# Performance work log

Measured on AMD Instinct MI355X. Metric: run time of the kernel, lower is better.

The kernel has to match this reference:

```python
import jax, jax.numpy as jnp
import numpy as np

B, P, S, H, R = 32, 512, 1024, 1024, 256


def setup_inputs() -> dict:
    key = jax.random.key(0)
    k1, k2, k3 = jax.random.split(key, 3)
    pairs = jax.random.randint(k1, (B, P, 2, 2), 0, S, dtype=jnp.int64 if jax.config.jax_enable_x64 else jnp.int32)
    hidden_states = jax.random.normal(k2, (B, S, H), dtype=jnp.float32)
    W = jax.random.normal(k3, (R, 3 * H), dtype=jnp.float32) * (1.0 / np.sqrt(3 * H))
    b = jnp.zeros((R,), dtype=jnp.float32)
    return {"pairs": pairs, "hidden_states": hidden_states, "W": W, "b": b}


def reference(pairs, hidden_states, W, b):
    # pairs: [B, P, 2, 2] -> [:, :, 0, :] = (h_start, h_end), [:, :, 1, :] = (t_start, t_end)
    def gather_tokens(idx):  # idx: [B, P] -> [B, P, H]
        return jnp.take_along_axis(hidden_states, idx[:, :, None], axis=1)

    head_embed = 0.5 * (gather_tokens(pairs[:, :, 0, 0]) + gather_tokens(pairs[:, :, 0, 1]))
    tail_embed = 0.5 * (gather_tokens(pairs[:, :, 1, 0]) + gather_tokens(pairs[:, :, 1, 1]))
    feats = jnp.concatenate([head_embed, tail_embed, head_embed * tail_embed], axis=-1)  # [B, P, 3H]
    logits = jnp.einsum('bpf,rf->bpr', feats, W) + b  # [B, P, R]
    return logits
```

## Files before the change

kernel.cpp:

```cpp
#include <hip/hip_runtime.h>

#define NB 32
#define NP 512
#define NS 1024
#define NH 1024
#define NR 256
#define K3 3072

#define BM 64
#define BK 64

typedef short short8 __attribute__((ext_vector_type(8)));
typedef short short4v __attribute__((ext_vector_type(4)));
typedef __bf16 bf16x8 __attribute__((ext_vector_type(8)));
typedef float f32x4 __attribute__((ext_vector_type(4)));

__device__ __forceinline__ unsigned short f2bf(float f) {
  unsigned u = __builtin_bit_cast(unsigned, f);
  u += 0x7fffu + ((u >> 16) & 1u);
  return (unsigned short)(u >> 16);
}

__device__ __forceinline__ f32x4 mfma_bf16(short8 a, short8 b, f32x4 c) {
  return __builtin_amdgcn_mfma_f32_16x16x32_bf16(
      __builtin_bit_cast(bf16x8, a), __builtin_bit_cast(bf16x8, b), c, 0, 0, 0);
}

__global__ void wconv_kernel(const float* __restrict__ W,
                             unsigned short* __restrict__ WbF) {
  int i = blockIdx.x * blockDim.x + threadIdx.x;
  int lane = i & 63, n16 = (i >> 6) & 15, kc = i >> 10;
  int lr = lane & 15, lg = lane >> 4;
  const float* src = W + (size_t)(n16 * 16 + lr) * K3 + kc * 32 + lg * 8;
  float4 a = *(const float4*)src;
  float4 b = *(const float4*)(src + 4);
  short8 o;
  o[0] = (short)f2bf(a.x); o[1] = (short)f2bf(a.y);
  o[2] = (short)f2bf(a.z); o[3] = (short)f2bf(a.w);
  o[4] = (short)f2bf(b.x); o[5] = (short)f2bf(b.y);
  o[6] = (short)f2bf(b.z); o[7] = (short)f2bf(b.w);
  *(short8*)(WbF + (size_t)i * 8) = o;
}

__global__ __launch_bounds__(512, 2) void gemm_kernel(
    const int* __restrict__ pairs, const float* __restrict__ hs,
    const unsigned short* __restrict__ WbF, const float* __restrict__ bias,
    float* __restrict__ out) {
  __shared__ __align__(16) unsigned short sA[2][3][BM][64];

  const int tid = threadIdx.x;
  const int blk = blockIdx.x;
  const int x     = blk & 7;
  const int jb    = blk >> 3;
  const int batch = x * 4 + (jb >> 3);
  const int mtile = jb & 7;
  const int m0    = (batch * 8 + mtile) * BM;

  const int pairi = tid >> 3;
  const int q     = tid & 7;
  int4 pr = ((const int4*)pairs)[m0 + pairi];
  const float* hb = hs + (size_t)batch * NS * NH;
  const float* rp[4];
  rp[0] = hb + (size_t)pr.x * NH + 4 * q;
  rp[1] = hb + (size_t)pr.y * NH + 4 * q;
  rp[2] = hb + (size_t)pr.z * NH + 4 * q;
  rp[3] = hb + (size_t)pr.w * NH + 4 * q;

  const int lane = tid & 63;
  const int w    = tid >> 6;
  const int lr   = lane & 15;
  const int lg   = lane >> 4;

  const unsigned short* wbase = WbF + (size_t)(w * 2) * 512 + (size_t)lane * 8;

  f32x4 acc[4][2];
#pragma unroll
  for (int i = 0; i < 4; ++i)
#pragma unroll
    for (int j = 0; j < 2; ++j) acc[i][j] = (f32x4){0.f, 0.f, 0.f, 0.f};

  float4 ld[8];
  short8 wcur[12], wnxt[12];

  auto load_w = [&](int s, short8* wd) {
#pragma unroll
    for (int part = 0; part < 3; ++part)
#pragma unroll
      for (int ks = 0; ks < 2; ++ks)
#pragma unroll
        for (int j = 0; j < 2; ++j)
          wd[part * 4 + ks * 2 + j] = *(const short8*)(
              wbase + (size_t)(part * 32 + s * 2 + ks) * 8192 + (size_t)j * 512);
  };

  auto load_gather = [&](int s) {
    const int o = s * BK;
#pragma unroll
    for (int jj = 0; jj < 8; ++jj)
      ld[jj] = *(const float4*)(rp[jj >> 1] + o + 32 * (jj & 1));
  };

  auto store_stage = [&](int buf) {
#pragma unroll
    for (int c = 0; c < 2; ++c) {
      short4v hv, tv, pv;
#pragma unroll
      for (int e = 0; e < 4; ++e) {
        float h = 0.5f * (((const float*)&ld[0 + c])[e] + ((const float*)&ld[2 + c])[e]);
        float t = 0.5f * (((const float*)&ld[4 + c])[e] + ((const float*)&ld[6 + c])[e]);
        float p = h * t;
        hv[e] = (short)f2bf(h); tv[e] = (short)f2bf(t); pv[e] = (short)f2bf(p);
      }
      const int chunkI = (q >> 1) + 4 * c;
      const int col = ((chunkI ^ (pairi & 7)) * 8) + (q & 1) * 4;
      *(short4v*)&sA[buf][0][pairi][col] = hv;
      *(short4v*)&sA[buf][1][pairi][col] = tv;
      *(short4v*)&sA[buf][2][pairi][col] = pv;
    }
  };

  auto compute = [&](int buf, short8* wc) {
#pragma unroll
    for (int ks = 0; ks < 2; ++ks) {
      short8 ah[4], at4[4], ap[4];
      const int col = (((ks * 4 + lg) ^ (lr & 7)) * 8);
#pragma unroll
      for (int i = 0; i < 4; ++i) {
        ah[i]  = *(const short8*)&sA[buf][0][i * 16 + lr][col];
        at4[i] = *(const short8*)&sA[buf][1][i * 16 + lr][col];
        ap[i]  = *(const short8*)&sA[buf][2][i * 16 + lr][col];
      }
#pragma unroll
      for (int j = 0; j < 2; ++j)
#pragma unroll
        for (int i = 0; i < 4; ++i) {
          acc[i][j] = mfma_bf16(ah[i],  wc[0 + ks * 2 + j], acc[i][j]);
          acc[i][j] = mfma_bf16(at4[i], wc[4 + ks * 2 + j], acc[i][j]);
          acc[i][j] = mfma_bf16(ap[i],  wc[8 + ks * 2 + j], acc[i][j]);
        }
    }
  };

  load_w(0, wcur);
  load_gather(0);
  store_stage(0);

  auto stage = [&](int s, short8* wc, short8* wn) {
    __syncthreads();
    const int buf = s & 1;
    if (s < 15) {
      load_w(s + 1, wn);
      load_gather(s + 1);
    }
    compute(buf, wc);
    if (s < 15) store_stage(buf ^ 1);
  };

#pragma unroll 1
  for (int sp = 0; sp < 8; ++sp) {
    stage(2 * sp,     wcur, wnxt);
    stage(2 * sp + 1, wnxt, wcur);
  }

#pragma unroll
  for (int j = 0; j < 2; ++j) {
    const int col  = w * 32 + j * 16 + lr;
    const float bv = bias[col];
#pragma unroll
    for (int i = 0; i < 4; ++i) {
      const size_t rbase = (size_t)(m0 + i * 16 + lg * 4) * NR + col;
#pragma unroll
      for (int r = 0; r < 4; ++r)
        out[rbase + (size_t)r * NR] = acc[i][j][r] + bv;
    }
  }
}

extern "C" void kernel_launch(void* const* d_in, const int* in_sizes, int n_in,
                              void* d_out, int out_size, void* d_ws, size_t ws_size,
                              hipStream_t stream) {
  const int*   pairs = (const int*)d_in[0];
  const float* hs    = (const float*)d_in[1];
  const float* W     = (const float*)d_in[2];
  const float* bias  = (const float*)d_in[3];
  float* out = (float*)d_out;
  unsigned short* WbF = (unsigned short*)d_ws;

  wconv_kernel<<<(96 * 16 * 64) / 256, 256, 0, stream>>>(W, WbF);
  gemm_kernel<<<(NB * NP) / BM, 512, 0, stream>>>(pairs, hs, WbF, bias, out);
}
```

Before: 231.9 us.

## Double threads per GEMM block and deepen gather prefetch to two stages

Each block now runs 1024 threads (16 waves) instead of 512, so every wave owns one 16-column N tile instead of two, and each thread gathers one float4 per row instead of two. This halves per-thread register use for accumulators and weight fragments. The gather is also prefetched two stages ahead using ping-ponged register buffers, to hide the latency of the random hidden-state loads. The cost is a heavier __syncthreads across 16 waves and each wave re-reading the shared-memory A tiles, which doubles LDS read traffic per MFMA.

Result: faster. 225.4 us (-2.8%).

```diff
diff --git a/kernel.cpp b/kernel.cpp
--- a/kernel.cpp
+++ b/kernel.cpp
@@ -42,7 +42,7 @@
   *(short8*)(WbF + (size_t)i * 8) = o;
 }
 
-__global__ __launch_bounds__(512, 2) void gemm_kernel(
+__global__ __launch_bounds__(1024, 4) void gemm_kernel(
     const int* __restrict__ pairs, const float* __restrict__ hs,
     const unsigned short* __restrict__ WbF, const float* __restrict__ bias,
     float* __restrict__ out) {
@@ -56,8 +56,8 @@
   const int mtile = jb & 7;
   const int m0    = (batch * 8 + mtile) * BM;
 
-  const int pairi = tid >> 3;
-  const int q     = tid & 7;
+  const int pairi = tid >> 4;
+  const int q     = tid & 15;
   int4 pr = ((const int4*)pairs)[m0 + pairi];
   const float* hb = hs + (size_t)batch * NS * NH;
   const float* rp[4];
@@ -71,52 +71,44 @@
   const int lr   = lane & 15;
   const int lg   = lane >> 4;
 
-  const unsigned short* wbase = WbF + (size_t)(w * 2) * 512 + (size_t)lane * 8;
+  const unsigned short* wbase = WbF + (size_t)w * 512 + (size_t)lane * 8;
 
-  f32x4 acc[4][2];
+  f32x4 acc[4];
 #pragma unroll
-  for (int i = 0; i < 4; ++i)
-#pragma unroll
-    for (int j = 0; j < 2; ++j) acc[i][j] = (f32x4){0.f, 0.f, 0.f, 0.f};
+  for (int i = 0; i < 4; ++i) acc[i] = (f32x4){0.f, 0.f, 0.f, 0.f};
 
-  float4 ld[8];
-  short8 wcur[12], wnxt[12];
+  float4 ldA[4], ldB[4];
+  short8 wcur[6], wnxt[6];
 
   auto load_w = [&](int s, short8* wd) {
 #pragma unroll
     for (int part = 0; part < 3; ++part)
 #pragma unroll
       for (int ks = 0; ks < 2; ++ks)
-#pragma unroll
-        for (int j = 0; j < 2; ++j)
-          wd[part * 4 + ks * 2 + j] = *(const short8*)(
-              wbase + (size_t)(part * 32 + s * 2 + ks) * 8192 + (size_t)j * 512);
+        wd[part * 2 + ks] = *(const short8*)(
+            wbase + (size_t)(part * 32 + s * 2 + ks) * 8192);
   };
 
-  auto load_gather = [&](int s) {
-    const int o = s * BK;
+  auto load_gather = [&](int s, float4* ld) {
 #pragma unroll
-    for (int jj = 0; jj < 8; ++jj)
-      ld[jj] = *(const float4*)(rp[jj >> 1] + o + 32 * (jj & 1));
+    for (int r = 0; r < 4; ++r)
+      ld[r] = *(const float4*)(rp[r] + s * BK);
   };
 
-  auto store_stage = [&](int buf) {
+  auto store_stage = [&](int buf, float4* ld) {
+    short4v hv, tv, pv;
 #pragma unroll
-    for (int c = 0; c < 2; ++c) {
-      short4v hv, tv, pv;
-#pragma unroll
-      for (int e = 0; e < 4; ++e) {
-        float h = 0.5f * (((const float*)&ld[0 + c])[e] + ((const float*)&ld[2 + c])[e]);
-        float t = 0.5f * (((const float*)&ld[4 + c])[e] + ((const float*)&ld[6 + c])[e]);
-        float p = h * t;
-        hv[e] = (short)f2bf(h); tv[e] = (short)f2bf(t); pv[e] = (short)f2bf(p);
-      }
-      const int chunkI = (q >> 1) + 4 * c;
-      const int col = ((chunkI ^ (pairi & 7)) * 8) + (q & 1) * 4;
-      *(short4v*)&sA[buf][0][pairi][col] = hv;
-      *(short4v*)&sA[buf][1][pairi][col] = tv;
-      *(short4v*)&sA[buf][2][pairi][col] = pv;
+    for (int e = 0; e < 4; ++e) {
+      float h = 0.5f * (((const float*)&ld[0])[e] + ((const float*)&ld[1])[e]);
+      float t = 0.5f * (((const float*)&ld[2])[e] + ((const float*)&ld[3])[e]);
+      float p = h * t;
+      hv[e] = (short)f2bf(h); tv[e] = (short)f2bf(t); pv[e] = (short)f2bf(p);
     }
+    const int chunkI = q >> 1;
+    const int col = ((chunkI ^ (pairi & 7)) * 8) + (q & 1) * 4;
+    *(short4v*)&sA[buf][0][pairi][col] = hv;
+    *(short4v*)&sA[buf][1][pairi][col] = tv;
+    *(short4v*)&sA[buf][2][pairi][col] = pv;
   };
 
   auto compute = [&](int buf, short8* wc) {
@@ -131,48 +123,41 @@
         ap[i]  = *(const short8*)&sA[buf][2][i * 16 + lr][col];
       }
 #pragma unroll
-      for (int j = 0; j < 2; ++j)
-#pragma unroll
-        for (int i = 0; i < 4; ++i) {
-          acc[i][j] = mfma_bf16(ah[i],  wc[0 + ks * 2 + j], acc[i][j]);
-          acc[i][j] = mfma_bf16(at4[i], wc[4 + ks * 2 + j], acc[i][j]);
-          acc[i][j] = mfma_bf16(ap[i],  wc[8 + ks * 2 + j], acc[i][j]);
-        }
+      for (int i = 0; i < 4; ++i) {
+        acc[i] = mfma_bf16(ah[i],  wc[0 + ks], acc[i]);
+        acc[i] = mfma_bf16(at4[i], wc[2 + ks], acc[i]);
+        acc[i] = mfma_bf16(ap[i],  wc[4 + ks], acc[i]);
+      }
     }
   };
 
+  load_gather(0, ldA);
   load_w(0, wcur);
-  load_gather(0);
-  store_stage(0);
+  store_stage(0, ldA);
+  load_gather(1, ldA);
 
-  auto stage = [&](int s, short8* wc, short8* wn) {
+  auto stage = [&](int s, short8* wc, short8* wn, float4* ldc, float4* ldn) {
     __syncthreads();
-    const int buf = s & 1;
-    if (s < 15) {
-      load_w(s + 1, wn);
-      load_gather(s + 1);
-    }
-    compute(buf, wc);
-    if (s < 15) store_stage(buf ^ 1);
+    if (s < 15) load_w(s + 1, wn);
+    if (s < 14) load_gather(s + 2, ldn);
+    compute(s & 1, wc);
+    if (s < 15) store_stage((s & 1) ^ 1, ldc);
   };
 
 #pragma unroll 1
   for (int sp = 0; sp < 8; ++sp) {
-    stage(2 * sp,     wcur, wnxt);
-    stage(2 * sp + 1, wnxt, wcur);
+    stage(2 * sp,     wcur, wnxt, ldA, ldB);
+    stage(2 * sp + 1, wnxt, wcur, ldB, ldA);
   }
 
+  const int col  = w * 16 + lr;
+  const float bv = bias[col];
 #pragma unroll
-  for (int j = 0; j < 2; ++j) {
-    const int col  = w * 32 + j * 16 + lr;
-    const float bv = bias[col];
+  for (int i = 0; i < 4; ++i) {
+    const size_t rbase = (size_t)(m0 + i * 16 + lg * 4) * NR + col;
 #pragma unroll
-    for (int i = 0; i < 4; ++i) {
-      const size_t rbase = (size_t)(m0 + i * 16 + lg * 4) * NR + col;
-#pragma unroll
-      for (int r = 0; r < 4; ++r)
-        out[rbase + (size_t)r * NR] = acc[i][j][r] + bv;
-    }
+    for (int r = 0; r < 4; ++r)
+      out[rbase + (size_t)r * NR] = acc[i][r] + bv;
   }
 }
 
@@ -187,5 +172,5 @@
   unsigned short* WbF = (unsigned short*)d_ws;
 
   wconv_kernel<<<(96 * 16 * 64) / 256, 256, 0, stream>>>(W, WbF);
-  gemm_kernel<<<(NB * NP) / BM, 512, 0, stream>>>(pairs, hs, WbF, bias, out);
+  gemm_kernel<<<(NB * NP) / BM, 1024, 0, stream>>>(pairs, hs, WbF, bias, out);
 }
```

## Split K across two thread groups per block with LDS reduction

Applied to the files above, without the earlier changes.

Doubles the block to 1024 threads split into two groups, each covering half of the hidden dimension with its own double-buffered LDS tiles, halving the serial stage count. Partial accumulators from the second group are reduced through LDS before the first group writes output with bias. The gather is reorganized to load 8 contiguous floats per thread and store full 8-wide bf16 vectors. This raises per-CU wave count for latency hiding but doubles LDS use and tightens the register budget under the new launch bounds, risking spills.

After: 369.9 us. 1.59x slower.

```diff
diff --git a/kernel.cpp b/kernel.cpp
--- a/kernel.cpp
+++ b/kernel.cpp
@@ -8,10 +8,8 @@
 #define K3 3072
 
 #define BM 64
-#define BK 64
 
 typedef short short8 __attribute__((ext_vector_type(8)));
-typedef short short4v __attribute__((ext_vector_type(4)));
 typedef __bf16 bf16x8 __attribute__((ext_vector_type(8)));
 typedef float f32x4 __attribute__((ext_vector_type(4)));
 
@@ -42,11 +40,11 @@
   *(short8*)(WbF + (size_t)i * 8) = o;
 }
 
-__global__ __launch_bounds__(512, 2) void gemm_kernel(
+__global__ __launch_bounds__(1024, 2) void gemm_kernel(
     const int* __restrict__ pairs, const float* __restrict__ hs,
     const unsigned short* __restrict__ WbF, const float* __restrict__ bias,
     float* __restrict__ out) {
-  __shared__ __align__(16) unsigned short sA[2][3][BM][64];
+  __shared__ __align__(16) unsigned short sA[2][2][3][BM][64];
 
   const int tid = threadIdx.x;
   const int blk = blockIdx.x;
@@ -56,22 +54,26 @@
   const int mtile = jb & 7;
   const int m0    = (batch * 8 + mtile) * BM;
 
-  const int pairi = tid >> 3;
-  const int q     = tid & 7;
+  const int g    = tid >> 9;
+  const int gtid = tid & 511;
+
+  const int pairi = gtid >> 3;
+  const int q     = gtid & 7;
   int4 pr = ((const int4*)pairs)[m0 + pairi];
-  const float* hb = hs + (size_t)batch * NS * NH;
+  const float* hb = hs + (size_t)batch * NS * NH + (size_t)g * 512 + q * 8;
   const float* rp[4];
-  rp[0] = hb + (size_t)pr.x * NH + 4 * q;
-  rp[1] = hb + (size_t)pr.y * NH + 4 * q;
-  rp[2] = hb + (size_t)pr.z * NH + 4 * q;
-  rp[3] = hb + (size_t)pr.w * NH + 4 * q;
+  rp[0] = hb + (size_t)pr.x * NH;
+  rp[1] = hb + (size_t)pr.y * NH;
+  rp[2] = hb + (size_t)pr.z * NH;
+  rp[3] = hb + (size_t)pr.w * NH;
 
   const int lane = tid & 63;
-  const int w    = tid >> 6;
+  const int wg   = (tid >> 6) & 7;
   const int lr   = lane & 15;
   const int lg   = lane >> 4;
 
-  const unsigned short* wbase = WbF + (size_t)(w * 2) * 512 + (size_t)lane * 8;
+  const unsigned short* wbase =
+      WbF + (size_t)(g * 16) * 8192 + (size_t)(wg * 2) * 512 + (size_t)lane * 8;
 
   f32x4 acc[4][2];
 #pragma unroll
@@ -94,29 +96,28 @@
   };
 
   auto load_gather = [&](int s) {
-    const int o = s * BK;
-#pragma unroll
-    for (int jj = 0; jj < 8; ++jj)
-      ld[jj] = *(const float4*)(rp[jj >> 1] + o + 32 * (jj & 1));
+    const int o = s * 64;
+#pragma unroll
+    for (int r = 0; r < 4; ++r) {
+      ld[2 * r]     = *(const float4*)(rp[r] + o);
+      ld[2 * r + 1] = *(const float4*)(rp[r] + o + 4);
+    }
   };
 
   auto store_stage = [&](int buf) {
-#pragma unroll
-    for (int c = 0; c < 2; ++c) {
-      short4v hv, tv, pv;
-#pragma unroll
-      for (int e = 0; e < 4; ++e) {
-        float h = 0.5f * (((const float*)&ld[0 + c])[e] + ((const float*)&ld[2 + c])[e]);
-        float t = 0.5f * (((const float*)&ld[4 + c])[e] + ((const float*)&ld[6 + c])[e]);
-        float p = h * t;
-        hv[e] = (short)f2bf(h); tv[e] = (short)f2bf(t); pv[e] = (short)f2bf(p);
-      }
-      const int chunkI = (q >> 1) + 4 * c;
-      const int col = ((chunkI ^ (pairi & 7)) * 8) + (q & 1) * 4;
-      *(short4v*)&sA[buf][0][pairi][col] = hv;
-      *(short4v*)&sA[buf][1][pairi][col] = tv;
-      *(short4v*)&sA[buf][2][pairi][col] = pv;
-    }
+    short8 hv, tv, pv;
+#pragma unroll
+    for (int e = 0; e < 8; ++e) {
+      const int hi = e >> 2, ei = e & 3;
+      float h = 0.5f * (((const float*)&ld[0 + hi])[ei] + ((const float*)&ld[2 + hi])[ei]);
+      float t = 0.5f * (((const float*)&ld[4 + hi])[ei] + ((const float*)&ld[6 + hi])[ei]);
+      float p = h * t;
+      hv[e] = (short)f2bf(h); tv[e] = (short)f2bf(t); pv[e] = (short)f2bf(p);
+    }
+    const int col = (q ^ (pairi & 7)) * 8;
+    *(short8*)&sA[g][buf][0][pairi][col] = hv;
+    *(short8*)&sA[g][buf][1][pairi][col] = tv;
+    *(short8*)&sA[g][buf][2][pairi][col] = pv;
   };
 
   auto compute = [&](int buf, short8* wc) {
@@ -126,9 +127,9 @@
       const int col = (((ks * 4 + lg) ^ (lr & 7)) * 8);
 #pragma unroll
       for (int i = 0; i < 4; ++i) {
-        ah[i]  = *(const short8*)&sA[buf][0][i * 16 + lr][col];
-        at4[i] = *(const short8*)&sA[buf][1][i * 16 + lr][col];
-        ap[i]  = *(const short8*)&sA[buf][2][i * 16 + lr][col];
+        ah[i]  = *(const short8*)&sA[g][buf][0][i * 16 + lr][col];
+        at4[i] = *(const short8*)&sA[g][buf][1][i * 16 + lr][col];
+        ap[i]  = *(const short8*)&sA[g][buf][2][i * 16 + lr][col];
       }
 #pragma unroll
       for (int j = 0; j < 2; ++j)
@@ -147,32 +148,46 @@
 
   auto stage = [&](int s, short8* wc, short8* wn) {
     __syncthreads();
-    const int buf = s & 1;
-    if (s < 15) {
+    if (s < 7) {
       load_w(s + 1, wn);
       load_gather(s + 1);
     }
-    compute(buf, wc);
-    if (s < 15) store_stage(buf ^ 1);
+    compute(s & 1, wc);
+    if (s < 7) store_stage((s & 1) ^ 1);
   };
 
 #pragma unroll 1
-  for (int sp = 0; sp < 8; ++sp) {
+  for (int sp = 0; sp < 4; ++sp) {
     stage(2 * sp,     wcur, wnxt);
     stage(2 * sp + 1, wnxt, wcur);
   }
 
-#pragma unroll
-  for (int j = 0; j < 2; ++j) {
-    const int col  = w * 32 + j * 16 + lr;
-    const float bv = bias[col];
-#pragma unroll
-    for (int i = 0; i < 4; ++i) {
-      const size_t rbase = (size_t)(m0 + i * 16 + lg * 4) * NR + col;
-#pragma unroll
-      for (int r = 0; r < 4; ++r)
-        out[rbase + (size_t)r * NR] = acc[i][j][r] + bv;
-    }
+  float* ldsF = (float*)&sA[0][0][0][0][0];
+  __syncthreads();
+  if (g == 1) {
+#pragma unroll
+    for (int i = 0; i < 4; ++i)
+#pragma unroll
+      for (int j = 0; j < 2; ++j) {
+        const int k = i * 2 + j;
+        *(f32x4*)&ldsF[(size_t)gtid * 32 + (size_t)((k ^ (gtid & 7)) * 4)] = acc[i][j];
+      }
+  }
+  __syncthreads();
+  if (g == 0) {
+#pragma unroll
+    for (int i = 0; i < 4; ++i)
+#pragma unroll
+      for (int j = 0; j < 2; ++j) {
+        const int k = i * 2 + j;
+        f32x4 o1 = *(const f32x4*)&ldsF[(size_t)gtid * 32 + (size_t)((k ^ (gtid & 7)) * 4)];
+        const int col  = wg * 32 + j * 16 + lr;
+        const float bv = bias[col];
+        const size_t rbase = (size_t)(m0 + i * 16 + lg * 4) * NR + col;
+#pragma unroll
+        for (int r = 0; r < 4; ++r)
+          out[rbase + (size_t)r * NR] = acc[i][j][r] + o1[r] + bv;
+      }
   }
 }
 
@@ -187,5 +202,5 @@
   unsigned short* WbF = (unsigned short*)d_ws;
 
   wconv_kernel<<<(96 * 16 * 64) / 256, 256, 0, stream>>>(W, WbF);
-  gemm_kernel<<<(NB * NP) / BM, 512, 0, stream>>>(pairs, hs, WbF, bias, out);
-}
+  gemm_kernel<<<(NB * NP) / BM, 1024, 0, stream>>>(pairs, hs, WbF, bias, out);
+}
```

## Deepen gather prefetch to four register stages and widen per-thread loads

Applied to the files above, without the earlier changes.

The gather of hidden-state rows is now software-pipelined four stages ahead using four rotating register buffers, instead of one stage ahead. Each thread now loads 8 contiguous floats per row, two adjacent float4s, and writes a single 16-byte swizzled LDS store per tensor. The aim is to hide the latency of the random-row global gathers behind more MFMA work. In exchange, register use rises sharply, so launch bounds drop to one block per SIMD pair, which lowers occupancy.

Result: slower. 283.1 us (+22.1%).

```diff
diff --git a/kernel.cpp b/kernel.cpp
--- a/kernel.cpp
+++ b/kernel.cpp
@@ -8,10 +8,8 @@
 #define K3 3072
 
 #define BM 64
-#define BK 64
 
 typedef short short8 __attribute__((ext_vector_type(8)));
-typedef short short4v __attribute__((ext_vector_type(4)));
 typedef __bf16 bf16x8 __attribute__((ext_vector_type(8)));
 typedef float f32x4 __attribute__((ext_vector_type(4)));
 
@@ -42,7 +40,7 @@
   *(short8*)(WbF + (size_t)i * 8) = o;
 }
 
-__global__ __launch_bounds__(512, 2) void gemm_kernel(
+__global__ __launch_bounds__(512, 1) void gemm_kernel(
     const int* __restrict__ pairs, const float* __restrict__ hs,
     const unsigned short* __restrict__ WbF, const float* __restrict__ bias,
     float* __restrict__ out) {
@@ -59,12 +57,12 @@
   const int pairi = tid >> 3;
   const int q     = tid & 7;
   int4 pr = ((const int4*)pairs)[m0 + pairi];
-  const float* hb = hs + (size_t)batch * NS * NH;
+  const float* hb = hs + (size_t)batch * NS * NH + 8 * q;
   const float* rp[4];
-  rp[0] = hb + (size_t)pr.x * NH + 4 * q;
-  rp[1] = hb + (size_t)pr.y * NH + 4 * q;
-  rp[2] = hb + (size_t)pr.z * NH + 4 * q;
-  rp[3] = hb + (size_t)pr.w * NH + 4 * q;
+  rp[0] = hb + (size_t)pr.x * NH;
+  rp[1] = hb + (size_t)pr.y * NH;
+  rp[2] = hb + (size_t)pr.z * NH;
+  rp[3] = hb + (size_t)pr.w * NH;
 
   const int lane = tid & 63;
   const int w    = tid >> 6;
@@ -79,7 +77,7 @@
 #pragma unroll
     for (int j = 0; j < 2; ++j) acc[i][j] = (f32x4){0.f, 0.f, 0.f, 0.f};
 
-  float4 ld[8];
+  float4 rgA[8], rgB[8], rgC[8], rgD[8];
   short8 wcur[12], wnxt[12];
 
   auto load_w = [&](int s, short8* wd) {
@@ -93,30 +91,29 @@
               wbase + (size_t)(part * 32 + s * 2 + ks) * 8192 + (size_t)j * 512);
   };
 
-  auto load_gather = [&](int s) {
-    const int o = s * BK;
+  auto load_gather = [&](int s, float4* ld) {
+    const int o = s * 64;
 #pragma unroll
-    for (int jj = 0; jj < 8; ++jj)
-      ld[jj] = *(const float4*)(rp[jj >> 1] + o + 32 * (jj & 1));
+    for (int r = 0; r < 4; ++r) {
+      ld[2 * r]     = *(const float4*)(rp[r] + o);
+      ld[2 * r + 1] = *(const float4*)(rp[r] + o + 4);
+    }
   };
 
-  auto store_stage = [&](int buf) {
+  auto store_stage = [&](int buf, const float4* ld) {
+    short8 hv, tv, pv;
 #pragma unroll
-    for (int c = 0; c < 2; ++c) {
-      short4v hv, tv, pv;
-#pragma unroll
-      for (int e = 0; e < 4; ++e) {
-        float h = 0.5f * (((const float*)&ld[0 + c])[e] + ((const float*)&ld[2 + c])[e]);
-        float t = 0.5f * (((const float*)&ld[4 + c])[e] + ((const float*)&ld[6 + c])[e]);
-        float p = h * t;
-        hv[e] = (short)f2bf(h); tv[e] = (short)f2bf(t); pv[e] = (short)f2bf(p);
-      }
-      const int chunkI = (q >> 1) + 4 * c;
-      const int col = ((chunkI ^ (pairi & 7)) * 8) + (q & 1) * 4;
-      *(short4v*)&sA[buf][0][pairi][col] = hv;
-      *(short4v*)&sA[buf][1][pairi][col] = tv;
-      *(short4v*)&sA[buf][2][pairi][col] = pv;
+    for (int e = 0; e < 8; ++e) {
+      const int hi = e >> 2, ei = e & 3;
+      float h = 0.5f * (((const float*)&ld[0 + hi])[ei] + ((const float*)&ld[2 + hi])[ei]);
+      float t = 0.5f * (((const float*)&ld[4 + hi])[ei] + ((const float*)&ld[6 + hi])[ei]);
+      float p = h * t;
+      hv[e] = (short)f2bf(h); tv[e] = (short)f2bf(t); pv[e] = (short)f2bf(p);
     }
+    const int col = (q ^ (pairi & 7)) * 8;
+    *(short8*)&sA[buf][0][pairi][col] = hv;
+    *(short8*)&sA[buf][1][pairi][col] = tv;
+    *(short8*)&sA[buf][2][pairi][col] = pv;
   };
 
   auto compute = [&](int buf, short8* wc) {
@@ -142,24 +139,29 @@
   };
 
   load_w(0, wcur);
-  load_gather(0);
-  store_stage(0);
+  load_gather(0, rgA);
+  load_gather(1, rgB);
+  load_gather(2, rgC);
+  load_gather(3, rgD);
+  store_stage(0, rgA);
+  load_gather(4, rgA);
 
-  auto stage = [&](int s, short8* wc, short8* wn) {
+  auto stage = [&](int s, short8* wc, short8* wn, float4* slot) {
     __syncthreads();
-    const int buf = s & 1;
+    if (s < 15) load_w(s + 1, wn);
+    compute(s & 1, wc);
     if (s < 15) {
-      load_w(s + 1, wn);
-      load_gather(s + 1);
+      store_stage((s & 1) ^ 1, slot);
+      if (s <= 10) load_gather(s + 5, slot);
     }
-    compute(buf, wc);
-    if (s < 15) store_stage(buf ^ 1);
   };
 
 #pragma unroll 1
-  for (int sp = 0; sp < 8; ++sp) {
-    stage(2 * sp,     wcur, wnxt);
-    stage(2 * sp + 1, wnxt, wcur);
+  for (int sp = 0; sp < 4; ++sp) {
+    stage(4 * sp + 0, wcur, wnxt, rgB);
+    stage(4 * sp + 1, wnxt, wcur, rgC);
+    stage(4 * sp + 2, wcur, wnxt, rgD);
+    stage(4 * sp + 3, wnxt, wcur, rgA);
   }
 
 #pragma unroll
```
